# Performance work log

Measured on AMD Instinct MI355X. Metric: run time of the kernel, lower is better.

Reference implementation:

```python
import jax, jax.numpy as jnp
import numpy as np
from jax.scipy.special import gammaln, logsumexp

T, K, D = 262144, 32, 64


def setup_inputs() -> dict:
    key = jax.random.key(0)
    ks = jax.random.split(key, 7)
    Y = jax.random.normal(ks[0], (T, D), dtype=jnp.float32)
    dT = jax.random.uniform(ks[1], (T,), dtype=jnp.float32) + 0.01  # strictly positive intervals
    A = jax.random.normal(ks[2], (K, K), dtype=jnp.float32)
    log_ab = jax.random.normal(ks[3], (K, 2), dtype=jnp.float32) * 0.5
    mu = jax.random.normal(ks[4], (K, D), dtype=jnp.float32)
    log_sigma = jax.random.normal(ks[5], (K, D), dtype=jnp.float32) * 0.1
    pi = jax.random.normal(ks[6], (K,), dtype=jnp.float32)
    return {"Y": Y, "dT": dT, "A": A, "log_ab": log_ab, "mu": mu, "log_sigma": log_sigma, "pi": pi}


def _gamma_ll(dT, log_ab):
    # per-state Gamma(concentration=exp(log_ab[:,0]), rate=exp(log_ab[:,1])) log_prob -> [T, K]
    a = jnp.exp(log_ab[:, 0])
    b = jnp.exp(log_ab[:, 1])
    const = a * log_ab[:, 1] - gammaln(a)  # a*log(b) - lgamma(a)
    return const[None, :] + jnp.log(dT)[:, None] * (a - 1.0)[None, :] - dT[:, None] * b[None, :]


def _gauss_ll(Y, mu, log_sigma):
    # diagonal-Gaussian emission log-likelihood summed over D, via GEMMs -> [T, K]
    inv_var = jnp.exp(-2.0 * log_sigma)  # [K, D]
    quad = (-0.5) * (Y * Y) @ inv_var.T + Y @ (mu * inv_var).T - 0.5 * jnp.sum(mu * mu * inv_var, axis=-1)[None, :]
    const = -jnp.sum(log_sigma, axis=-1) - 0.5 * D * jnp.log(2.0 * jnp.pi).astype(Y.dtype)
    return quad + const[None, :]


def _hmm_lognorm(pi0, logA, ll):
    # log-domain forward algorithm; returns log normalizer (scalar)
    alpha0 = pi0 + ll[0]

    def step(alpha, ll_t):
        # alpha_t[j] = logsumexp_i(alpha[i] + logA[i, j]) + ll_t[j]
        alpha = logsumexp(alpha[:, None] + logA, axis=0) + ll_t
        return alpha, None

    alphaT, _ = jax.lax.scan(step, alpha0, ll[1:])
    return logsumexp(alphaT)


def reference(Y, dT, A, log_ab, mu, log_sigma, pi):
    h = Y  # obs_model embedding (identity for Gaussian emission model)
    y_ll = _gauss_ll(Y, mu, log_sigma)          # [T, K]
    y_loss = jnp.zeros((), dtype=Y.dtype)
    dT_ll = _gamma_ll(dT, log_ab)               # [T, K]
    ll = y_ll + dT_ll
    logA = jax.nn.log_softmax(A, axis=1)        # LogSoftmax(dim=1)(A)
    pi0 = jax.nn.log_softmax(pi, axis=0)        # LogSoftmax(dim=0)(pi)
    loss = -1.0 * _hmm_lognorm(pi0, logA, ll) + y_loss
    return h, loss
```

## Files before the change

kernel.cpp:

```cpp
#include <hip/hip_runtime.h>
#include <stdint.h>

#define TT 262144
#define KK 32
#define DD 64
#define LSTEP 32
#define PCH 8192

typedef __attribute__((ext_vector_type(4)))  float f4v;
typedef __attribute__((ext_vector_type(16))) float f16v;
typedef __attribute__((ext_vector_type(4)))  short s4v;
typedef __attribute__((ext_vector_type(8)))  short s8v;
typedef __attribute__((ext_vector_type(8)))  __bf16 bf8v;
typedef __attribute__((ext_vector_type(2)))  unsigned int u2v;
typedef __attribute__((ext_vector_type(4)))  unsigned int u4v;

#define WS_AFRAG_US 0
#define WS_WFRAG_US 1024
#define WS_WF    2560
#define WS_CK    6656
#define WS_AM1   6688
#define WS_BB    6720
#define WS_PI0   6752
#define WS_LS    8192
#define WS_LS2   16384
#define SH_MATS  33280
#define SH_MATS2 (33280 + PCH*1024)
#define LN2F 0.69314718055994531f

__device__ __forceinline__ unsigned pkbf(float hi, float lo) {
    return __builtin_amdgcn_perm(__builtin_bit_cast(unsigned, hi),
                                 __builtin_bit_cast(unsigned, lo), 0x07060302u);
}
__device__ __forceinline__ unsigned short f2bf_rne(float f) {
    unsigned u = __builtin_bit_cast(unsigned, f);
    unsigned r = u + 0x7FFFu + ((u >> 16) & 1u);
    return (unsigned short)(r >> 16);
}
__device__ __forceinline__ float bf2f(unsigned short u) {
    return __builtin_bit_cast(float, (unsigned)u << 16);
}
__device__ __forceinline__ float wmax32(float v) {
    v = fmaxf(v, __shfl_xor(v, 1));  v = fmaxf(v, __shfl_xor(v, 2));
    v = fmaxf(v, __shfl_xor(v, 4));  v = fmaxf(v, __shfl_xor(v, 8));
    v = fmaxf(v, __shfl_xor(v, 16));
    return v;
}
__device__ __forceinline__ float wmax64(float v) {
    v = wmax32(v); v = fmaxf(v, __shfl_xor(v, 32));
    return v;
}
__device__ __forceinline__ float wsum32(float v) {
    v += __shfl_xor(v, 1); v += __shfl_xor(v, 2); v += __shfl_xor(v, 4);
    v += __shfl_xor(v, 8); v += __shfl_xor(v, 16);
    return v;
}
__device__ __forceinline__ float wsum64(float v) {
    v = wsum32(v); v += __shfl_xor(v, 32);
    return v;
}
__device__ __forceinline__ float wval(int dd, int k, const float* mu, const float* lsg) {
    int d = dd & 63;
    float lv = lsg[k * DD + d];
    float iv = __expf(-2.f * lv);
    return (dd < DD) ? (-0.5f * iv) : (mu[k * DD + d] * iv);
}
__device__ __forceinline__ f16v mfma16(s8v a, s8v b, f16v c) {
    return __builtin_amdgcn_mfma_f32_32x32x16_bf16(
        __builtin_bit_cast(bf8v, a), __builtin_bit_cast(bf8v, b), c, 0, 0, 0);
}

__global__ void k0_prep(const float* __restrict__ Y, const float* __restrict__ A,
                        const float* __restrict__ lab, const float* __restrict__ mu,
                        const float* __restrict__ lsg, const float* __restrict__ pi,
                        float* __restrict__ ws, float* __restrict__ out)
{
    __shared__ float lseA[KK];
    const int tid = threadIdx.x;
    if (tid < KK) {
        float m = -1e30f;
        for (int j = 0; j < KK; ++j) m = fmaxf(m, A[tid * KK + j]);
        float s = 0.f;
        for (int j = 0; j < KK; ++j) s += __expf(A[tid * KK + j] - m);
        lseA[tid] = m + __logf(s);

        float mp = -1e30f;
        for (int j = 0; j < KK; ++j) mp = fmaxf(mp, pi[j]);
        float sp = 0.f;
        for (int j = 0; j < KK; ++j) sp += __expf(pi[j] - mp);
        ws[WS_PI0 + tid] = pi[tid] - (mp + __logf(sp));

        float la = lab[tid * 2 + 0], lb = lab[tid * 2 + 1];
        float a = __expf(la), b = __expf(lb);
        float c1 = 0.f, c2 = 0.f;
        for (int d = 0; d < DD; ++d) {
            float lv = lsg[tid * DD + d];
            float mv = mu[tid * DD + d];
            c1 -= lv;
            c2 += mv * mv * __expf(-2.f * lv);
        }
        ws[WS_CK + tid]  = a * lb - lgammaf(a) + c1 - 0.5f * c2 - 32.f * 1.8378770664093453f;
        ws[WS_AM1 + tid] = a - 1.f;
        ws[WS_BB + tid]  = b;
    }
    __syncthreads();
    unsigned short* us = (unsigned short*)ws;
    for (int idx = tid; idx < 1024; idx += 256) {
        int g2 = idx >> 9, rem = idx & 511, ln = rem >> 3, e = rem & 7;
        int m = 16 * g2 + 8 * (e >> 2) + 4 * (ln >> 5) + (e & 3), i = ln & 31;
        us[WS_AFRAG_US + idx] = f2bf_rne(__expf(A[m * KK + i] - lseA[m]));
    }
    for (int idx = tid; idx < 4096; idx += 256) {
        int s2 = idx >> 9, rem = idx & 511, ln = rem >> 3, e = rem & 7;
        int dd = 16 * s2 + 8 * (e >> 2) + 4 * (ln >> 5) + (e & 3);
        us[WS_WFRAG_US + idx] = f2bf_rne(wval(dd, ln & 31, mu, lsg));
    }
    for (int idx = tid; idx < 4096; idx += 256) {
        int dd = idx >> 5, k = idx & 31;
        ws[WS_WF + idx] = wval(dd, k, mu, lsg);
    }
    if (tid < DD) out[tid] = Y[tid];
}

__global__ __launch_bounds__(256, 4) void k1_scan(
    const float* __restrict__ Y, const float* __restrict__ dTp,
    float* __restrict__ ws, float* __restrict__ out)
{
    __shared__ __align__(16) float Ebuf[4][2][1152];
    __shared__ __align__(16) float dtv[4][64], dtl[4][64];

    const int tid = threadIdx.x;
    const int wv = tid >> 6, l = tid & 63, h = l >> 5, c = l & 31;
    const int pA = (blockIdx.x * 4 + wv) * 2;
    const int pB = pA + 1;
    const int t0A = 1 + pA * LSTEP;
    const int t0B = t0A + LSTEP;

    const unsigned short* afr = (const unsigned short*)ws + WS_AFRAG_US;
    const unsigned short* wfr = (const unsigned short*)ws + WS_WFRAG_US;

    const float cK = ws[WS_CK + c], am1 = ws[WS_AM1 + c], bb = ws[WS_BB + c];

    {
        int t = t0A + l;
        float dv = (t < TT) ? dTp[t] : 1.f;
        dtv[wv][l] = dv;
        dtl[wv][l] = __logf(dv);
    }

    f16v zf;
    #pragma unroll
    for (int r = 0; r < 16; ++r) zf[r] = 0.f;

    {
        const size_t gbase = (size_t)t0A * DD;
        #pragma unroll
        for (int i = 0; i < 16; ++i) {
            const size_t gi = gbase + (size_t)i * 256 + l * 4;
            if (gi < (size_t)TT * DD) {
                f4v y4 = *(const f4v*)(Y + gi);
                *(f4v*)(out + gi) = y4;
            }
        }
    }

    s8v wfv[8];
    #pragma unroll
    for (int s2 = 0; s2 < 8; ++s2) wfv[s2] = *(const s8v*)(wfr + s2 * 512 + l * 8);

    auto emit = [&](int t0) -> f16v {
        f16v acc = zf;
        s8v raws[4];
        const bool ok = (t0 + c) < TT;
        const float* yrow = Y + (size_t)(t0 + c) * DD;
        #pragma unroll
        for (int g2 = 0; g2 < 4; ++g2) {
            f4v y0, y1;
            y0[0]=0.f; y0[1]=0.f; y0[2]=0.f; y0[3]=0.f;
            y1[0]=0.f; y1[1]=0.f; y1[2]=0.f; y1[3]=0.f;
            if (ok) {
                y0 = *(const f4v*)(yrow + 16 * g2 + 4 * h);
                y1 = *(const f4v*)(yrow + 16 * g2 + 8 + 4 * h);
            }
            const f4v q0 = y0 * y0, q1 = y1 * y1;
            u4v sqp, rwp;
            sqp[0] = pkbf(q0[1], q0[0]); sqp[1] = pkbf(q0[3], q0[2]);
            sqp[2] = pkbf(q1[1], q1[0]); sqp[3] = pkbf(q1[3], q1[2]);
            rwp[0] = pkbf(y0[1], y0[0]); rwp[1] = pkbf(y0[3], y0[2]);
            rwp[2] = pkbf(y1[1], y1[0]); rwp[3] = pkbf(y1[3], y1[2]);
            raws[g2] = __builtin_bit_cast(s8v, rwp);
            acc = mfma16(__builtin_bit_cast(s8v, sqp), wfv[g2], acc);
        }
        #pragma unroll
        for (int g2 = 0; g2 < 4; ++g2)
            acc = mfma16(raws[g2], wfv[4 + g2], acc);
        return acc;
    };

    const f16v accA = emit(t0A);
    const f16v accB = emit(t0B);

    const s8v aF0 = *(const s8v*)(afr + l * 8);
    const s8v aF1 = *(const s8v*)(afr + 512 + l * 8);

    auto llphase = [&](const f16v& acc, int ch, int nsteps) -> float {
        float csv = 0.f;
        float* E = &Ebuf[wv][ch][0];
        #pragma unroll
        for (int m = 0; m < 4; ++m) {
            const f4v dv4 = *(const f4v*)(&dtv[wv][ch * 32 + 8 * m + 4 * h]);
            const f4v dl4 = *(const f4v*)(&dtl[wv][ch * 32 + 8 * m + 4 * h]);
            #pragma unroll
            for (int j = 0; j < 4; ++j) {
                const int row = 8 * m + 4 * h + j;
                float llv = acc[4 * m + j] + cK + am1 * dl4[j] - bb * dv4[j];
                float cm = wmax32(llv);
                E[row * 36 + c] = __expf(llv - cm);
                csv += (row < nsteps) ? cm : 0.f;
            }
        }
        return wsum64(csv) * (1.f / 32.f);
    };
    const int nsB = (pB == PCH - 1) ? (TT - t0B) : LSTEP;
    const float caccA = llphase(accA, 0, LSTEP);
    const float caccB = llphase(accB, 1, nsB);

    asm volatile("s_waitcnt lgkmcnt(0)" ::: "memory");

    f16v SA, SB;
    #pragma unroll
    for (int m = 0; m < 4; ++m)
        #pragma unroll
        for (int j = 0; j < 4; ++j) {
            const float id = ((8 * m + 4 * h + j) == c) ? 1.f : 0.f;
            SA[4 * m + j] = id;
            SB[4 * m + j] = id;
        }
    float l2A = 0.f, l2B = 0.f;
    const float* EA = &Ebuf[wv][0][0];
    const float* EB = &Ebuf[wv][1][0];

    auto step = [&](f16v& S, const float* E, int n) {
        u4v b0, b1;
        b0[0] = pkbf(S[1],  S[0]);  b0[1] = pkbf(S[3],  S[2]);
        b0[2] = pkbf(S[5],  S[4]);  b0[3] = pkbf(S[7],  S[6]);
        b1[0] = pkbf(S[9],  S[8]);  b1[1] = pkbf(S[11], S[10]);
        b1[2] = pkbf(S[13], S[12]); b1[3] = pkbf(S[15], S[14]);
        f16v Dv = mfma16(aF0, __builtin_bit_cast(s8v, b0), zf);
        Dv = mfma16(aF1, __builtin_bit_cast(s8v, b1), Dv);
        #pragma unroll
        for (int m = 0; m < 4; ++m) {
            const f4v e4 = *(const f4v*)(E + n * 36 + 8 * m + 4 * h);
            S[4 * m + 0] = Dv[4 * m + 0] * e4[0];
            S[4 * m + 1] = Dv[4 * m + 1] * e4[1];
            S[4 * m + 2] = Dv[4 * m + 2] * e4[2];
            S[4 * m + 3] = Dv[4 * m + 3] * e4[3];
        }
    };
    auto rescale = [&](f16v& S, float& l2) {
        float mx = S[0];
        #pragma unroll
        for (int r = 1; r < 16; ++r) mx = fmaxf(mx, S[r]);
        mx = wmax64(mx);
        const float inv = __fdividef(1.f, mx);
        #pragma unroll
        for (int r = 0; r < 16; ++r) S[r] *= inv;
        l2 += __log2f(mx);
    };

    if (pB != PCH - 1) {
        #pragma unroll
        for (int n = 0; n < LSTEP; ++n) {
            step(SA, EA, n);
            step(SB, EB, n);
            if ((n & 3) == 3) { rescale(SA, l2A); rescale(SB, l2B); }
        }
    } else {
        for (int n = 0; n < LSTEP; ++n) {
            step(SA, EA, n);
            if (n < nsB) step(SB, EB, n);
            if ((n & 3) == 3) { rescale(SA, l2A); rescale(SB, l2B); }
        }
    }

    auto storemat = [&](const f16v& S, int ch, int p, float cacc, float l2) {
        unsigned short* Tb = (unsigned short*)&Ebuf[wv][ch][0];
        asm volatile("s_waitcnt lgkmcnt(0)" ::: "memory");
        #pragma unroll
        for (int m = 0; m < 4; ++m)
            #pragma unroll
            for (int j = 0; j < 4; ++j)
                Tb[(8 * m + 4 * h + j) * 36 + c] = f2bf_rne(S[4 * m + j]);
        asm volatile("s_waitcnt lgkmcnt(0)" ::: "memory");
        u2v tg0 = *(const u2v*)(Tb + c * 36 + 0  + 4 * h);
        u2v tg1 = *(const u2v*)(Tb + c * 36 + 8  + 4 * h);
        u2v tg2 = *(const u2v*)(Tb + c * 36 + 16 + 4 * h);
        u2v tg3 = *(const u2v*)(Tb + c * 36 + 24 + 4 * h);
        unsigned short* gm = (unsigned short*)ws + SH_MATS + (size_t)p * 1024 + l * 16;
        u4v s0; s0[0] = tg0[0]; s0[1] = tg0[1]; s0[2] = tg1[0]; s0[3] = tg1[1];
        u4v s1; s1[0] = tg2[0]; s1[1] = tg2[1]; s1[2] = tg3[0]; s1[3] = tg3[1];
        *(u4v*)(gm) = s0;
        *(u4v*)(gm + 8) = s1;
        if (l == 0) ws[WS_LS + p] = cacc + LN2F * l2;
    };
    storemat(SA, 0, pA, caccA, l2A);
    storemat(SB, 1, pB, caccB, l2B);
}

__device__ __forceinline__ f16v prodAU(const u4v a0, const u4v a1, const f16v U, const f16v zf) {
    u4v b0, b1;
    b0[0] = pkbf(U[1],  U[0]);  b0[1] = pkbf(U[3],  U[2]);
    b0[2] = pkbf(U[5],  U[4]);  b0[3] = pkbf(U[7],  U[6]);
    b1[0] = pkbf(U[9],  U[8]);  b1[1] = pkbf(U[11], U[10]);
    b1[2] = pkbf(U[13], U[12]); b1[3] = pkbf(U[15], U[14]);
    f16v Dv = mfma16(__builtin_bit_cast(s8v, a0), __builtin_bit_cast(s8v, b0), zf);
    Dv = mfma16(__builtin_bit_cast(s8v, a1), __builtin_bit_cast(s8v, b1), Dv);
    return Dv;
}

__global__ __launch_bounds__(128, 1) void k2_combine(float* __restrict__ ws)
{
    __shared__ __align__(16) unsigned short slot[2][1152];
    __shared__ float scl[2], lac[2];
    const int tid = threadIdx.x, wv = tid >> 6, l = tid & 63, h = l >> 5, c = l & 31;
    const int blk = blockIdx.x;
    const int idx0 = blk * 64 + wv * 32;
    const unsigned short* mats = (const unsigned short*)ws + SH_MATS;

    float lsv = (l < 32) ? ws[WS_LS + idx0 + l] : 0.f;
    float lssum = wsum64(lsv);

    f16v zf;
    #pragma unroll
    for (int r = 0; r < 16; ++r) zf[r] = 0.f;
    f16v U;
    #pragma unroll
    for (int m = 0; m < 4; ++m)
        #pragma unroll
        for (int j = 0; j < 4; ++j)
            U[4 * m + j] = ((8 * m + 4 * h + j) == c) ? 1.f : 0.f;
    float l2a = 0.f;

    u4v pf[2][2];
    {
        const u4v* mp0 = (const u4v*)(mats + (size_t)idx0 * 1024) + l * 2;
        const u4v* mp1 = (const u4v*)(mats + (size_t)(idx0 + 1) * 1024) + l * 2;
        pf[0][0] = mp0[0]; pf[0][1] = mp0[1];
        pf[1][0] = mp1[0]; pf[1][1] = mp1[1];
    }
    for (int q = 0; q < 32; ++q) {
        const u4v a0 = pf[q & 1][0], a1 = pf[q & 1][1];
        if (q + 2 < 32) {
            const u4v* mp = (const u4v*)(mats + (size_t)(idx0 + q + 2) * 1024) + l * 2;
            pf[q & 1][0] = mp[0]; pf[q & 1][1] = mp[1];
        }
        f16v Dv = prodAU(a0, a1, U, zf);
        if ((q & 3) == 3) {
            float mx = Dv[0];
            #pragma unroll
            for (int r = 1; r < 16; ++r) mx = fmaxf(mx, Dv[r]);
            mx = wmax64(mx);
            const float inv = __fdividef(1.f, mx);
            #pragma unroll
            for (int r = 0; r < 16; ++r) U[r] = Dv[r] * inv;
            l2a += __log2f(mx);
        } else {
            U = Dv;
        }
    }
    #pragma unroll
    for (int m = 0; m < 4; ++m)
        #pragma unroll
        for (int j = 0; j < 4; ++j)
            slot[wv][(8 * m + 4 * h + j) * 36 + c] = f2bf_rne(U[4 * m + j]);
    if (l == 0) { scl[wv] = lssum; lac[wv] = l2a; }
    __syncthreads();

    if (wv == 0) {
        u4v a0, a1;
        {
            u2v t0 = *(const u2v*)(&slot[1][c * 36 + 0 + 4 * h]);
            u2v t1 = *(const u2v*)(&slot[1][c * 36 + 8 + 4 * h]);
            u2v t2 = *(const u2v*)(&slot[1][c * 36 + 16 + 4 * h]);
            u2v t3 = *(const u2v*)(&slot[1][c * 36 + 24 + 4 * h]);
            a0[0] = t0[0]; a0[1] = t0[1]; a0[2] = t1[0]; a0[3] = t1[1];
            a1[0] = t2[0]; a1[1] = t2[1]; a1[2] = t3[0]; a1[3] = t3[1];
        }
        f16v Dv = prodAU(a0, a1, U, zf);
        float mx = Dv[0];
        #pragma unroll
        for (int r = 1; r < 16; ++r) mx = fmaxf(mx, Dv[r]);
        mx = wmax64(mx);
        const float inv = __fdividef(1.f, mx);
        #pragma unroll
        for (int r = 0; r < 16; ++r) U[r] = Dv[r] * inv;
        const float l2tot = lac[0] + lac[1] + __log2f(mx);
        asm volatile("s_waitcnt lgkmcnt(0)" ::: "memory");
        #pragma unroll
        for (int m = 0; m < 4; ++m)
            #pragma unroll
            for (int j = 0; j < 4; ++j)
                slot[0][(8 * m + 4 * h + j) * 36 + c] = f2bf_rne(U[4 * m + j]);
        asm volatile("s_waitcnt lgkmcnt(0)" ::: "memory");
        u2v tg[4];
        #pragma unroll
        for (int g = 0; g < 4; ++g)
            tg[g] = *(const u2v*)(&slot[0][c * 36 + 8 * g + 4 * h]);
        unsigned short* gm = (unsigned short*)ws + SH_MATS2 + (size_t)blk * 1024 + l * 16;
        u4v s0; s0[0] = tg[0][0]; s0[1] = tg[0][1]; s0[2] = tg[1][0]; s0[3] = tg[1][1];
        u4v s1; s1[0] = tg[2][0]; s1[1] = tg[2][1]; s1[2] = tg[3][0]; s1[3] = tg[3][1];
        *(u4v*)(gm) = s0;
        *(u4v*)(gm + 8) = s1;
        if (l == 0) ws[WS_LS2 + blk] = scl[0] + scl[1] + LN2F * l2tot;
    }
}

__global__ __launch_bounds__(1024, 1) void k3_final(
    const float* __restrict__ Y, const float* __restrict__ dTp,
    float* __restrict__ ws, float* __restrict__ out)
{
    __shared__ __align__(16) unsigned short slot[16][1152];
    __shared__ float sc[16];
    const int tid = threadIdx.x, wv = tid >> 6, l = tid & 63, h = l >> 5, c = l & 31;
    const unsigned short* mats2 = (const unsigned short*)ws + SH_MATS2;

    f16v zf;
    #pragma unroll
    for (int r = 0; r < 16; ++r) zf[r] = 0.f;

    const int idx0 = wv * 8;
    float lsv = (l < 8) ? ws[WS_LS2 + idx0 + l] : 0.f;
    float lssum = wsum64(lsv);
    f16v U;
    #pragma unroll
    for (int m = 0; m < 4; ++m)
        #pragma unroll
        for (int j = 0; j < 4; ++j)
            U[4 * m + j] = ((8 * m + 4 * h + j) == c) ? 1.f : 0.f;
    float l2a = 0.f;
    u4v pf[2][2];
    {
        const u4v* mp0 = (const u4v*)(mats2 + (size_t)idx0 * 1024) + l * 2;
        const u4v* mp1 = (const u4v*)(mats2 + (size_t)(idx0 + 1) * 1024) + l * 2;
        pf[0][0] = mp0[0]; pf[0][1] = mp0[1];
        pf[1][0] = mp1[0]; pf[1][1] = mp1[1];
    }
    for (int q = 0; q < 8; ++q) {
        const u4v a0 = pf[q & 1][0], a1 = pf[q & 1][1];
        if (q + 2 < 8) {
            const u4v* mp = (const u4v*)(mats2 + (size_t)(idx0 + q + 2) * 1024) + l * 2;
            pf[q & 1][0] = mp[0]; pf[q & 1][1] = mp[1];
        }
        f16v Dv = prodAU(a0, a1, U, zf);
        if ((q & 3) == 3) {
            float mx = Dv[0];
            #pragma unroll
            for (int r = 1; r < 16; ++r) mx = fmaxf(mx, Dv[r]);
            mx = wmax64(mx);
            const float inv = __fdividef(1.f, mx);
            #pragma unroll
            for (int r = 0; r < 16; ++r) U[r] = Dv[r] * inv;
            l2a += __log2f(mx);
        } else {
            U = Dv;
        }
    }
    #pragma unroll
    for (int m = 0; m < 4; ++m)
        #pragma unroll
        for (int j = 0; j < 4; ++j)
            slot[wv][(8 * m + 4 * h + j) * 36 + c] = f2bf_rne(U[4 * m + j]);
    if (l == 0) sc[wv] = lssum + LN2F * l2a;
    __syncthreads();

    for (int s = 1; s < 16; s <<= 1) {
        const int cnt = 16 / (2 * s);
        if (wv < cnt) {
            const int i = wv * 2 * s;
            s8v aA0, aA1, bB0, bB1;
            {
                u2v t0 = *(const u2v*)(&slot[i + s][c * 36 + 0 + 4 * h]);
                u2v t1 = *(const u2v*)(&slot[i + s][c * 36 + 8 + 4 * h]);
                u2v t2 = *(const u2v*)(&slot[i + s][c * 36 + 16 + 4 * h]);
                u2v t3 = *(const u2v*)(&slot[i + s][c * 36 + 24 + 4 * h]);
                u4v a0; a0[0] = t0[0]; a0[1] = t0[1]; a0[2] = t1[0]; a0[3] = t1[1];
                u4v a1; a1[0] = t2[0]; a1[1] = t2[1]; a1[2] = t3[0]; a1[3] = t3[1];
                aA0 = __builtin_bit_cast(s8v, a0);
                aA1 = __builtin_bit_cast(s8v, a1);
                #pragma unroll
                for (int j = 0; j < 4; ++j) {
                    bB0[j]     = (short)slot[i][(0  + 4 * h + j) * 36 + c];
                    bB0[4 + j] = (short)slot[i][(8  + 4 * h + j) * 36 + c];
                    bB1[j]     = (short)slot[i][(16 + 4 * h + j) * 36 + c];
                    bB1[4 + j] = (short)slot[i][(24 + 4 * h + j) * 36 + c];
                }
            }
            f16v Dv = mfma16(aA0, bB0, zf);
            Dv = mfma16(aA1, bB1, Dv);
            float mx = Dv[0];
            #pragma unroll
            for (int r = 1; r < 16; ++r) mx = fmaxf(mx, Dv[r]);
            mx = wmax64(mx);
            const float inv = __fdividef(1.f, mx);
            #pragma unroll
            for (int m = 0; m < 4; ++m)
                #pragma unroll
                for (int j = 0; j < 4; ++j)
                    slot[i][(8 * m + 4 * h + j) * 36 + c] = f2bf_rne(Dv[4 * m + j] * inv);
            if (l == 0) sc[i] = sc[i] + sc[i + s] + __logf(mx);
        }
        __syncthreads();
    }

    if (wv == 0) {
        float acc = 0.f;
        const float* Wf = ws + WS_WF;
        for (int dd = 0; dd < 128; ++dd) {
            const float yv = Y[dd & 63];
            const float f = (dd < 64) ? yv * yv : yv;
            acc = fmaf(f, Wf[dd * 32 + c], acc);
        }
        const float dt0 = dTp[0];
        const float ll0 = acc + ws[WS_CK + c] + ws[WS_AM1 + c] * __logf(dt0) - ws[WS_BB + c] * dt0;
        const float av = ws[WS_PI0 + c] + ll0;
        const float c0 = wmax32(av);
        const float a0 = __expf(av - c0);
        float part = 0.f;
        #pragma unroll
        for (int i = 0; i < 16; ++i) {
            const int ii = 16 * h + i;
            const float m = bf2f(slot[0][c * 36 + ii]);
            const float ai = __shfl(a0, ii);
            part = fmaf(m, ai, part);
        }
        const float srow = part + __shfl_xor(part, 32);
        const float tot = wsum32(srow);
        if (l == 0) out[(size_t)TT * DD] = -(sc[0] + c0 + __logf(tot));
    }
}

extern "C" void kernel_launch(void* const* d_in, const int* in_sizes, int n_in,
                              void* d_out, int out_size, void* d_ws, size_t ws_size,
                              hipStream_t stream)
{
    const float* Y   = (const float*)d_in[0];
    const float* dTp = (const float*)d_in[1];
    const float* A   = (const float*)d_in[2];
    const float* lab = (const float*)d_in[3];
    const float* mu  = (const float*)d_in[4];
    const float* lsg = (const float*)d_in[5];
    const float* pi  = (const float*)d_in[6];
    float* out = (float*)d_out;
    float* ws  = (float*)d_ws;

    hipLaunchKernelGGL(k0_prep, dim3(1), dim3(256), 0, stream, Y, A, lab, mu, lsg, pi, ws, out);
    hipLaunchKernelGGL(k1_scan, dim3(PCH / 8), dim3(256), 0, stream, Y, dTp, ws, out);
    hipLaunchKernelGGL(k2_combine, dim3(128), dim3(128), 0, stream, ws);
    hipLaunchKernelGGL(k3_final, dim3(1), dim3(1024), 0, stream, Y, dTp, ws, out);
}
```

Baseline: 199.0 us.

## Give each wave one chunk, staging Y through LDS and doubling grid size

```diff
diff --git a/kernel.cpp b/kernel.cpp
--- a/kernel.cpp
+++ b/kernel.cpp
@@ -6,6 +6,7 @@
 #define DD 64
 #define LSTEP 32
 #define PCH 8192
+#define YSTRIDE 68
 
 typedef __attribute__((ext_vector_type(4)))  float f4v;
 typedef __attribute__((ext_vector_type(16))) float f16v;
@@ -126,23 +127,22 @@
     const float* __restrict__ Y, const float* __restrict__ dTp,
     float* __restrict__ ws, float* __restrict__ out)
 {
-    __shared__ __align__(16) float Ebuf[4][2][1152];
-    __shared__ __align__(16) float dtv[4][64], dtl[4][64];
+    __shared__ __align__(16) float Yt[4][32 * YSTRIDE];
+    __shared__ __align__(16) float dtv[4][32], dtl[4][32];
 
     const int tid = threadIdx.x;
     const int wv = tid >> 6, l = tid & 63, h = l >> 5, c = l & 31;
-    const int pA = (blockIdx.x * 4 + wv) * 2;
-    const int pB = pA + 1;
-    const int t0A = 1 + pA * LSTEP;
-    const int t0B = t0A + LSTEP;
+    const int p = blockIdx.x * 4 + wv;
+    const int t0 = 1 + p * LSTEP;
+    const int nsteps = min(LSTEP, TT - t0);
 
     const unsigned short* afr = (const unsigned short*)ws + WS_AFRAG_US;
     const unsigned short* wfr = (const unsigned short*)ws + WS_WFRAG_US;
 
     const float cK = ws[WS_CK + c], am1 = ws[WS_AM1 + c], bb = ws[WS_BB + c];
 
-    {
-        int t = t0A + l;
+    if (l < 32) {
+        int t = t0 + l;
         float dv = (t < TT) ? dTp[t] : 1.f;
         dtv[wv][l] = dv;
         dtl[wv][l] = __logf(dv);
@@ -153,94 +153,72 @@
     for (int r = 0; r < 16; ++r) zf[r] = 0.f;
 
     {
-        const size_t gbase = (size_t)t0A * DD;
-        #pragma unroll
-        for (int i = 0; i < 16; ++i) {
+        const size_t gbase = (size_t)t0 * DD;
+        const int r = (l >> 4);
+        const int col = (l & 15) * 4;
+        #pragma unroll
+        for (int i = 0; i < 8; ++i) {
             const size_t gi = gbase + (size_t)i * 256 + l * 4;
-            if (gi < (size_t)TT * DD) {
-                f4v y4 = *(const f4v*)(Y + gi);
-                *(f4v*)(out + gi) = y4;
-            }
-        }
-    }
-
-    s8v wfv[8];
-    #pragma unroll
-    for (int s2 = 0; s2 < 8; ++s2) wfv[s2] = *(const s8v*)(wfr + s2 * 512 + l * 8);
-
-    auto emit = [&](int t0) -> f16v {
-        f16v acc = zf;
-        s8v raws[4];
-        const bool ok = (t0 + c) < TT;
-        const float* yrow = Y + (size_t)(t0 + c) * DD;
-        #pragma unroll
-        for (int g2 = 0; g2 < 4; ++g2) {
-            f4v y0, y1;
-            y0[0]=0.f; y0[1]=0.f; y0[2]=0.f; y0[3]=0.f;
-            y1[0]=0.f; y1[1]=0.f; y1[2]=0.f; y1[3]=0.f;
-            if (ok) {
-                y0 = *(const f4v*)(yrow + 16 * g2 + 4 * h);
-                y1 = *(const f4v*)(yrow + 16 * g2 + 8 + 4 * h);
-            }
-            const f4v q0 = y0 * y0, q1 = y1 * y1;
-            u4v sqp, rwp;
-            sqp[0] = pkbf(q0[1], q0[0]); sqp[1] = pkbf(q0[3], q0[2]);
-            sqp[2] = pkbf(q1[1], q1[0]); sqp[3] = pkbf(q1[3], q1[2]);
-            rwp[0] = pkbf(y0[1], y0[0]); rwp[1] = pkbf(y0[3], y0[2]);
-            rwp[2] = pkbf(y1[1], y1[0]); rwp[3] = pkbf(y1[3], y1[2]);
-            raws[g2] = __builtin_bit_cast(s8v, rwp);
-            acc = mfma16(__builtin_bit_cast(s8v, sqp), wfv[g2], acc);
-        }
-        #pragma unroll
-        for (int g2 = 0; g2 < 4; ++g2)
-            acc = mfma16(raws[g2], wfv[4 + g2], acc);
-        return acc;
-    };
-
-    const f16v accA = emit(t0A);
-    const f16v accB = emit(t0B);
+            f4v y4; y4[0] = 0.f; y4[1] = 0.f; y4[2] = 0.f; y4[3] = 0.f;
+            const bool ok = gi < (size_t)TT * DD;
+            if (ok) y4 = *(const f4v*)(Y + gi);
+            if (ok) *(f4v*)(out + gi) = y4;
+            *(f4v*)(&Yt[wv][(i * 4 + r) * YSTRIDE + col]) = y4;
+        }
+    }
+
+    f16v acc = zf;
+    s8v raws[4];
+    #pragma unroll
+    for (int g2 = 0; g2 < 4; ++g2) {
+        const f4v y0 = *(const f4v*)(&Yt[wv][c * YSTRIDE + 16 * g2 + 4 * h]);
+        const f4v y1 = *(const f4v*)(&Yt[wv][c * YSTRIDE + 16 * g2 + 8 + 4 * h]);
+        const f4v q0 = y0 * y0, q1 = y1 * y1;
+        u4v sqp, rwp;
+        sqp[0] = pkbf(q0[1], q0[0]); sqp[1] = pkbf(q0[3], q0[2]);
+        sqp[2] = pkbf(q1[1], q1[0]); sqp[3] = pkbf(q1[3], q1[2]);
+        rwp[0] = pkbf(y0[1], y0[0]); rwp[1] = pkbf(y0[3], y0[2]);
+        rwp[2] = pkbf(y1[1], y1[0]); rwp[3] = pkbf(y1[3], y1[2]);
+        raws[g2] = __builtin_bit_cast(s8v, rwp);
+        s8v wf = *(const s8v*)(wfr + g2 * 512 + l * 8);
+        acc = mfma16(__builtin_bit_cast(s8v, sqp), wf, acc);
+    }
+    #pragma unroll
+    for (int g2 = 0; g2 < 4; ++g2) {
+        s8v wf = *(const s8v*)(wfr + (4 + g2) * 512 + l * 8);
+        acc = mfma16(raws[g2], wf, acc);
+    }
 
     const s8v aF0 = *(const s8v*)(afr + l * 8);
     const s8v aF1 = *(const s8v*)(afr + 512 + l * 8);
 
-    auto llphase = [&](const f16v& acc, int ch, int nsteps) -> float {
-        float csv = 0.f;
-        float* E = &Ebuf[wv][ch][0];
-        #pragma unroll
-        for (int m = 0; m < 4; ++m) {
-            const f4v dv4 = *(const f4v*)(&dtv[wv][ch * 32 + 8 * m + 4 * h]);
-            const f4v dl4 = *(const f4v*)(&dtl[wv][ch * 32 + 8 * m + 4 * h]);
-            #pragma unroll
-            for (int j = 0; j < 4; ++j) {
-                const int row = 8 * m + 4 * h + j;
-                float llv = acc[4 * m + j] + cK + am1 * dl4[j] - bb * dv4[j];
-                float cm = wmax32(llv);
-                E[row * 36 + c] = __expf(llv - cm);
-                csv += (row < nsteps) ? cm : 0.f;
-            }
-        }
-        return wsum64(csv) * (1.f / 32.f);
-    };
-    const int nsB = (pB == PCH - 1) ? (TT - t0B) : LSTEP;
-    const float caccA = llphase(accA, 0, LSTEP);
-    const float caccB = llphase(accB, 1, nsB);
+    float csv = 0.f;
+    #pragma unroll
+    for (int m = 0; m < 4; ++m) {
+        const f4v dv4 = *(const f4v*)(&dtv[wv][8 * m + 4 * h]);
+        const f4v dl4 = *(const f4v*)(&dtl[wv][8 * m + 4 * h]);
+        #pragma unroll
+        for (int j = 0; j < 4; ++j) {
+            const int row = 8 * m + 4 * h + j;
+            float llv = acc[4 * m + j] + cK + am1 * dl4[j] - bb * dv4[j];
+            float cm = wmax32(llv);
+            Yt[wv][row * YSTRIDE + c] = __expf(llv - cm);
+            csv += (row < nsteps) ? cm : 0.f;
+        }
+    }
+    float cacc = wsum64(csv) * (1.f / 32.f);
 
     asm volatile("s_waitcnt lgkmcnt(0)" ::: "memory");
 
-    f16v SA, SB;
+    f16v S;
     #pragma unroll
     for (int m = 0; m < 4; ++m)
         #pragma unroll
-        for (int j = 0; j < 4; ++j) {
-            const float id = ((8 * m + 4 * h + j) == c) ? 1.f : 0.f;
-            SA[4 * m + j] = id;
-            SB[4 * m + j] = id;
-        }
-    float l2A = 0.f, l2B = 0.f;
-    const float* EA = &Ebuf[wv][0][0];
-    const float* EB = &Ebuf[wv][1][0];
-
-    auto step = [&](f16v& S, const float* E, int n) {
+        for (int j = 0; j < 4; ++j)
+            S[4 * m + j] = ((8 * m + 4 * h + j) == c) ? 1.f : 0.f;
+    float l2acc = 0.f;
+
+    auto step = [&](int n) {
         u4v b0, b1;
         b0[0] = pkbf(S[1],  S[0]);  b0[1] = pkbf(S[3],  S[2]);
         b0[2] = pkbf(S[5],  S[4]);  b0[3] = pkbf(S[7],  S[6]);
@@ -250,14 +228,14 @@
         Dv = mfma16(aF1, __builtin_bit_cast(s8v, b1), Dv);
         #pragma unroll
         for (int m = 0; m < 4; ++m) {
-            const f4v e4 = *(const f4v*)(E + n * 36 + 8 * m + 4 * h);
+            const f4v e4 = *(const f4v*)(&Yt[wv][n * YSTRIDE + 8 * m + 4 * h]);
             S[4 * m + 0] = Dv[4 * m + 0] * e4[0];
             S[4 * m + 1] = Dv[4 * m + 1] * e4[1];
             S[4 * m + 2] = Dv[4 * m + 2] * e4[2];
             S[4 * m + 3] = Dv[4 * m + 3] * e4[3];
         }
     };
-    auto rescale = [&](f16v& S, float& l2) {
+    auto rescale = [&]() {
         float mx = S[0];
         #pragma unroll
         for (int r = 1; r < 16; ++r) mx = fmaxf(mx, S[r]);
@@ -265,46 +243,40 @@
         const float inv = __fdividef(1.f, mx);
         #pragma unroll
         for (int r = 0; r < 16; ++r) S[r] *= inv;
-        l2 += __log2f(mx);
+        l2acc += __log2f(mx);
     };
 
-    if (pB != PCH - 1) {
+    if (p != PCH - 1) {
         #pragma unroll
         for (int n = 0; n < LSTEP; ++n) {
-            step(SA, EA, n);
-            step(SB, EB, n);
-            if ((n & 3) == 3) { rescale(SA, l2A); rescale(SB, l2B); }
+            step(n);
+            if ((n & 3) == 3) rescale();
         }
     } else {
-        for (int n = 0; n < LSTEP; ++n) {
-            step(SA, EA, n);
-            if (n < nsB) step(SB, EB, n);
-            if ((n & 3) == 3) { rescale(SA, l2A); rescale(SB, l2B); }
-        }
-    }
-
-    auto storemat = [&](const f16v& S, int ch, int p, float cacc, float l2) {
-        unsigned short* Tb = (unsigned short*)&Ebuf[wv][ch][0];
-        asm volatile("s_waitcnt lgkmcnt(0)" ::: "memory");
-        #pragma unroll
-        for (int m = 0; m < 4; ++m)
-            #pragma unroll
-            for (int j = 0; j < 4; ++j)
-                Tb[(8 * m + 4 * h + j) * 36 + c] = f2bf_rne(S[4 * m + j]);
-        asm volatile("s_waitcnt lgkmcnt(0)" ::: "memory");
-        u2v tg0 = *(const u2v*)(Tb + c * 36 + 0  + 4 * h);
-        u2v tg1 = *(const u2v*)(Tb + c * 36 + 8  + 4 * h);
-        u2v tg2 = *(const u2v*)(Tb + c * 36 + 16 + 4 * h);
-        u2v tg3 = *(const u2v*)(Tb + c * 36 + 24 + 4 * h);
-        unsigned short* gm = (unsigned short*)ws + SH_MATS + (size_t)p * 1024 + l * 16;
-        u4v s0; s0[0] = tg0[0]; s0[1] = tg0[1]; s0[2] = tg1[0]; s0[3] = tg1[1];
-        u4v s1; s1[0] = tg2[0]; s1[1] = tg2[1]; s1[2] = tg3[0]; s1[3] = tg3[1];
-        *(u4v*)(gm) = s0;
-        *(u4v*)(gm + 8) = s1;
-        if (l == 0) ws[WS_LS + p] = cacc + LN2F * l2;
-    };
-    storemat(SA, 0, pA, caccA, l2A);
-    storemat(SB, 1, pB, caccB, l2B);
+        for (int n = 0; n < nsteps; ++n) {
+            step(n);
+            if ((n & 3) == 3) rescale();
+        }
+    }
+
+    unsigned short* Tb = (unsigned short*)&Yt[wv][0];
+    asm volatile("s_waitcnt lgkmcnt(0)" ::: "memory");
+    #pragma unroll
+    for (int m = 0; m < 4; ++m)
+        #pragma unroll
+        for (int j = 0; j < 4; ++j)
+            Tb[(8 * m + 4 * h + j) * 36 + c] = f2bf_rne(S[4 * m + j]);
+    asm volatile("s_waitcnt lgkmcnt(0)" ::: "memory");
+    u2v tg0 = *(const u2v*)(Tb + c * 36 + 0  + 4 * h);
+    u2v tg1 = *(const u2v*)(Tb + c * 36 + 8  + 4 * h);
+    u2v tg2 = *(const u2v*)(Tb + c * 36 + 16 + 4 * h);
+    u2v tg3 = *(const u2v*)(Tb + c * 36 + 24 + 4 * h);
+    unsigned short* gm = (unsigned short*)ws + SH_MATS + (size_t)p * 1024 + l * 16;
+    u4v s0; s0[0] = tg0[0]; s0[1] = tg0[1]; s0[2] = tg1[0]; s0[3] = tg1[1];
+    u4v s1; s1[0] = tg2[0]; s1[1] = tg2[1]; s1[2] = tg3[0]; s1[3] = tg3[1];
+    *(u4v*)(gm) = s0;
+    *(u4v*)(gm + 8) = s1;
+    if (l == 0) ws[WS_LS + p] = cacc + LN2F * l2acc;
 }
 
 __device__ __forceinline__ f16v prodAU(const u4v a0, const u4v a1, const f16v U, const f16v zf) {
@@ -554,7 +526,7 @@
     float* ws  = (float*)d_ws;
 
     hipLaunchKernelGGL(k0_prep, dim3(1), dim3(256), 0, stream, Y, A, lab, mu, lsg, pi, ws, out);
-    hipLaunchKernelGGL(k1_scan, dim3(PCH / 8), dim3(256), 0, stream, Y, dTp, ws, out);
+    hipLaunchKernelGGL(k1_scan, dim3(PCH / 4), dim3(256), 0, stream, Y, dTp, ws, out);
     hipLaunchKernelGGL(k2_combine, dim3(128), dim3(128), 0, stream, ws);
     hipLaunchKernelGGL(k3_final, dim3(1), dim3(1024), 0, stream, Y, dTp, ws, out);
 }
```

Result: faster. 188.4 us (-5.3%).

## Stage Y as bf16 in LDS during copy pass instead of re-reading global

Applied to the files above, without the earlier changes.

```diff
diff --git a/kernel.cpp b/kernel.cpp
--- a/kernel.cpp
+++ b/kernel.cpp
@@ -126,15 +126,15 @@
     const float* __restrict__ Y, const float* __restrict__ dTp,
     float* __restrict__ ws, float* __restrict__ out)
 {
-    __shared__ __align__(16) float Ebuf[4][2][1152];
+    __shared__ __align__(16) float Ebuf[4][2304];
     __shared__ __align__(16) float dtv[4][64], dtl[4][64];
 
     const int tid = threadIdx.x;
     const int wv = tid >> 6, l = tid & 63, h = l >> 5, c = l & 31;
-    const int pA = (blockIdx.x * 4 + wv) * 2;
-    const int pB = pA + 1;
+    const int p2 = blockIdx.x * 4 + wv;
+    const int pA = p2 * 2, pB = pA + 1;
     const int t0A = 1 + pA * LSTEP;
-    const int t0B = t0A + LSTEP;
+    const int nsB = (p2 == PCH / 2 - 1) ? (TT - (t0A + LSTEP)) : LSTEP;
 
     const unsigned short* afr = (const unsigned short*)ws + WS_AFRAG_US;
     const unsigned short* wfr = (const unsigned short*)ws + WS_WFRAG_US;
@@ -152,64 +152,68 @@
     #pragma unroll
     for (int r = 0; r < 16; ++r) zf[r] = 0.f;
 
+    unsigned short* Ybase = (unsigned short*)&Ebuf[wv][0];
+    float* Ewave = &Ebuf[wv][0];
+
     {
         const size_t gbase = (size_t)t0A * DD;
+        const int rr = l & 3, cb = l >> 2;
+        const int g2s = cb >> 2, bs = (cb >> 1) & 1, hs = cb & 1;
         #pragma unroll
         for (int i = 0; i < 16; ++i) {
-            const size_t gi = gbase + (size_t)i * 256 + l * 4;
-            if (gi < (size_t)TT * DD) {
-                f4v y4 = *(const f4v*)(Y + gi);
-                *(f4v*)(out + gi) = y4;
+            const size_t gi = gbase + (size_t)i * 256 + (size_t)(rr * 64 + cb * 4);
+            f4v y4; y4[0] = 0.f; y4[1] = 0.f; y4[2] = 0.f; y4[3] = 0.f;
+            const bool ok = gi < (size_t)TT * DD;
+            if (ok) y4 = *(const f4v*)(Y + gi);
+            if (ok) *(f4v*)(out + gi) = y4;
+            const int r = i * 4 + rr;
+            const int off = (i >> 3) * 2304 + g2s * 512 + (32 * hs + (r & 31)) * 8 + 4 * bs;
+            u2v pw; pw[0] = pkbf(y4[1], y4[0]); pw[1] = pkbf(y4[3], y4[2]);
+            *(u2v*)(Ybase + off) = pw;
+        }
+    }
+    asm volatile("s_waitcnt lgkmcnt(0)" ::: "memory");
+
+    auto emit = [&](int ch) -> f16v {
+        const unsigned short* Yb = Ybase + ch * 2304;
+        f16v a = zf;
+        s8v raws[4];
+        #pragma unroll
+        for (int g2 = 0; g2 < 4; ++g2) {
+            const s8v yf = *(const s8v*)(Yb + g2 * 512 + l * 8);
+            raws[g2] = yf;
+            u4v qp;
+            #pragma unroll
+            for (int e2 = 0; e2 < 4; ++e2) {
+                const float f0 = bf2f((unsigned short)yf[2 * e2]);
+                const float f1 = bf2f((unsigned short)yf[2 * e2 + 1]);
+                qp[e2] = pkbf(f1 * f1, f0 * f0);
             }
-        }
-    }
-
-    s8v wfv[8];
-    #pragma unroll
-    for (int s2 = 0; s2 < 8; ++s2) wfv[s2] = *(const s8v*)(wfr + s2 * 512 + l * 8);
-
-    auto emit = [&](int t0) -> f16v {
-        f16v acc = zf;
-        s8v raws[4];
-        const bool ok = (t0 + c) < TT;
-        const float* yrow = Y + (size_t)(t0 + c) * DD;
+            const s8v wf = *(const s8v*)(wfr + g2 * 512 + l * 8);
+            a = mfma16(__builtin_bit_cast(s8v, qp), wf, a);
+        }
         #pragma unroll
         for (int g2 = 0; g2 < 4; ++g2) {
-            f4v y0, y1;
-            y0[0]=0.f; y0[1]=0.f; y0[2]=0.f; y0[3]=0.f;
-            y1[0]=0.f; y1[1]=0.f; y1[2]=0.f; y1[3]=0.f;
-            if (ok) {
-                y0 = *(const f4v*)(yrow + 16 * g2 + 4 * h);
-                y1 = *(const f4v*)(yrow + 16 * g2 + 8 + 4 * h);
-            }
-            const f4v q0 = y0 * y0, q1 = y1 * y1;
-            u4v sqp, rwp;
-            sqp[0] = pkbf(q0[1], q0[0]); sqp[1] = pkbf(q0[3], q0[2]);
-            sqp[2] = pkbf(q1[1], q1[0]); sqp[3] = pkbf(q1[3], q1[2]);
-            rwp[0] = pkbf(y0[1], y0[0]); rwp[1] = pkbf(y0[3], y0[2]);
-            rwp[2] = pkbf(y1[1], y1[0]); rwp[3] = pkbf(y1[3], y1[2]);
-            raws[g2] = __builtin_bit_cast(s8v, rwp);
-            acc = mfma16(__builtin_bit_cast(s8v, sqp), wfv[g2], acc);
-        }
-        #pragma unroll
-        for (int g2 = 0; g2 < 4; ++g2)
-            acc = mfma16(raws[g2], wfv[4 + g2], acc);
-        return acc;
+            const s8v wf = *(const s8v*)(wfr + (4 + g2) * 512 + l * 8);
+            a = mfma16(raws[g2], wf, a);
+        }
+        return a;
     };
-
-    const f16v accA = emit(t0A);
-    const f16v accB = emit(t0B);
+    const f16v accA = emit(0);
+    const f16v accB = emit(1);
 
     const s8v aF0 = *(const s8v*)(afr + l * 8);
     const s8v aF1 = *(const s8v*)(afr + 512 + l * 8);
 
     auto llphase = [&](const f16v& acc, int ch, int nsteps) -> float {
+        float* E = Ewave + ch * 1152;
+        const float* dv = &dtv[wv][ch * 32];
+        const float* dl = &dtl[wv][ch * 32];
         float csv = 0.f;
-        float* E = &Ebuf[wv][ch][0];
         #pragma unroll
         for (int m = 0; m < 4; ++m) {
-            const f4v dv4 = *(const f4v*)(&dtv[wv][ch * 32 + 8 * m + 4 * h]);
-            const f4v dl4 = *(const f4v*)(&dtl[wv][ch * 32 + 8 * m + 4 * h]);
+            const f4v dv4 = *(const f4v*)(dv + 8 * m + 4 * h);
+            const f4v dl4 = *(const f4v*)(dl + 8 * m + 4 * h);
             #pragma unroll
             for (int j = 0; j < 4; ++j) {
                 const int row = 8 * m + 4 * h + j;
@@ -221,7 +225,6 @@
         }
         return wsum64(csv) * (1.f / 32.f);
     };
-    const int nsB = (pB == PCH - 1) ? (TT - t0B) : LSTEP;
     const float caccA = llphase(accA, 0, LSTEP);
     const float caccB = llphase(accB, 1, nsB);
 
@@ -237,8 +240,8 @@
             SB[4 * m + j] = id;
         }
     float l2A = 0.f, l2B = 0.f;
-    const float* EA = &Ebuf[wv][0][0];
-    const float* EB = &Ebuf[wv][1][0];
+    const float* EA = Ewave;
+    const float* EB = Ewave + 1152;
 
     auto step = [&](f16v& S, const float* E, int n) {
         u4v b0, b1;
@@ -268,7 +271,7 @@
         l2 += __log2f(mx);
     };
 
-    if (pB != PCH - 1) {
+    if (p2 != PCH / 2 - 1) {
         #pragma unroll
         for (int n = 0; n < LSTEP; ++n) {
             step(SA, EA, n);
@@ -284,7 +287,7 @@
     }
 
     auto storemat = [&](const f16v& S, int ch, int p, float cacc, float l2) {
-        unsigned short* Tb = (unsigned short*)&Ebuf[wv][ch][0];
+        unsigned short* Tb = (unsigned short*)(Ewave + ch * 1152);
         asm volatile("s_waitcnt lgkmcnt(0)" ::: "memory");
         #pragma unroll
         for (int m = 0; m < 4; ++m)
```

Result: faster. 194.4 us (-2.3%).
